# Optimization experiments

Hardware: AMD Instinct MI355X
Metric: run time of the kernel (lower is better)

## Reference

```python
import jax, jax.numpy as jnp
import numpy as np

B, N, I, O, R = 8, 1024, 256, 256, 8


def setup_inputs() -> dict:
    key = jax.random.key(0)
    k1, k2, k3 = jax.random.split(key, 3)
    x = jax.random.normal(k1, (B, N, I), dtype=jnp.float32)
    adj = jax.random.uniform(k2, (B, N, N, R), dtype=jnp.float32)  # soft adjacency [b, src, dst, r]
    weight = jax.random.normal(k3, (R, I, O), dtype=jnp.float32)   # per-relation transform
    return {"x": x, "adj": adj, "weight": weight}


def reference(x, adj, weight):
    # per-relation transformed features: [b, src, r, o]
    f = jnp.einsum('bni,rio->bnro', x, weight)
    # contraction over source nodes and relations, weighted by soft adjacency:
    # out[b, dst, o] = sum_{src, r} adj[b, src, dst, r] * f[b, src, r, o]
    out = jnp.einsum('bnro,bnmr->bmo', f, adj)
    # normalization: total incoming soft-edge weight per destination node
    denom = jnp.clip(adj.sum(axis=(1, 3)), 1e-16, None)  # [b, dst]
    return out / denom[..., None]
```

## Files before the change

kernel.cpp:

```cpp
#include <hip/hip_runtime.h>
#include <hip/hip_bf16.h>
#include <stdint.h>


typedef float          floatx4  __attribute__((ext_vector_type(4)));
typedef short          shortx8  __attribute__((ext_vector_type(8)));
typedef unsigned short ushortx4 __attribute__((ext_vector_type(4)));
typedef unsigned short ushortx8 __attribute__((ext_vector_type(8)));

__device__ __forceinline__ unsigned short f2bf(float f) {
  __hip_bfloat16 h = __float2bfloat16(f);
  unsigned short u; __builtin_memcpy(&u, &h, 2);
  return u;
}

__device__ __forceinline__ void gload16(const void* g, void* l) {
  __builtin_amdgcn_global_load_lds((__attribute__((address_space(1))) void*)g,
                                   (__attribute__((address_space(3))) void*)l,
                                   16, 0, 0);
}

__global__ __launch_bounds__(256) void prep_xw(const float* __restrict__ x,
                                               const float* __restrict__ w,
                                               unsigned short* __restrict__ xbf,
                                               unsigned short* __restrict__ wt) {
  int bid = blockIdx.x;
  if (bid < 1024) {
    int t = bid * 256 + threadIdx.x;
    const float4* p = (const float4*)x + (size_t)t * 2;
    float4 a = p[0], b4 = p[1];
    ushortx8 o;
    o[0] = f2bf(a.x);  o[1] = f2bf(a.y);  o[2] = f2bf(a.z);  o[3] = f2bf(a.w);
    o[4] = f2bf(b4.x); o[5] = f2bf(b4.y); o[6] = f2bf(b4.z); o[7] = f2bf(b4.w);
    *(ushortx8*)(xbf + (size_t)t * 8) = o;
  } else {
    int id = (bid - 1024) * 256 + threadIdx.x;
    int r = id >> 16, i = (id >> 8) & 255, o = id & 255;
    float v = w[((size_t)(r * 256 + i) << 8) + o];
    wt[((size_t)(o * 8 + r) << 8) + i] = f2bf(v);
  }
}

__global__ __launch_bounds__(256) void k1_gemm(const unsigned short* __restrict__ xbf,
                                               const unsigned short* __restrict__ wt,
                                               unsigned short* __restrict__ ft) {
  int bid = blockIdx.x;
  int p0 = (bid & 15) * 128, q0 = (bid >> 4) * 128;
  int l = threadIdx.x & 63, w = threadIdx.x >> 6;
  int lr = l & 15, lg = l >> 4;
  int pw = p0 + (w >> 1) * 64, qw = q0 + (w & 1) * 64;

  floatx4 acc[4][4] = {};
#pragma unroll
  for (int ks = 0; ks < 8; ++ks) {
    shortx8 a[4], b[4];
#pragma unroll
    for (int pi = 0; pi < 4; ++pi)
      a[pi] = *(const shortx8*)(wt + (size_t)(pw + pi * 16 + lr) * 256 + ks * 32 + lg * 8);
#pragma unroll
    for (int qi = 0; qi < 4; ++qi)
      b[qi] = *(const shortx8*)(xbf + (size_t)(qw + qi * 16 + lr) * 256 + ks * 32 + lg * 8);
#pragma unroll
    for (int pi = 0; pi < 4; ++pi)
#pragma unroll
      for (int qi = 0; qi < 4; ++qi)
        acc[pi][qi] = __builtin_amdgcn_mfma_f32_16x16x32_bf16(a[pi], b[qi], acc[pi][qi], 0, 0, 0);
  }
#pragma unroll
  for (int pi = 0; pi < 4; ++pi) {
    int nbase = pw + pi * 16 + lg * 4;
    int o = nbase >> 3, rb = nbase & 7;
#pragma unroll
    for (int qi = 0; qi < 4; ++qi) {
      int m = qw + qi * 16 + lr;
      int b8 = m >> 10, src = m & 1023;
      ushortx4 h;
      h[0] = f2bf(acc[pi][qi][0]); h[1] = f2bf(acc[pi][qi][1]);
      h[2] = f2bf(acc[pi][qi][2]); h[3] = f2bf(acc[pi][qi][3]);
      *(ushortx4*)(ft + ((size_t)(b8 * 256 + o) << 13) + src * 8 + rb) = h;
    }
  }
}

#define ASZ 4096
#define BSZ (128 * 64)
__global__ __launch_bounds__(512, 4) void k2_gemm(const float* __restrict__ adj,
                                                  const unsigned short* __restrict__ ft,
                                                  float* __restrict__ pout,
                                                  float* __restrict__ dpart) {
  __shared__ __align__(16) unsigned short Alds[2 * ASZ];
  __shared__ __align__(16) unsigned short Blds[4 * BSZ];

  int bid = blockIdx.x;
  int b = bid & 7;
  int o0 = ((bid >> 3) & 1) * 128;
  int kc = (bid >> 4) & 1;
  int dst0 = (bid >> 5) * 64;

  int t = threadIdx.x, l = t & 63, w = t >> 6;
  int lr = l & 15, lg = l >> 4;
  int wm = w >> 2, wo = w & 3;

  int dst_l = (t >> 1) & 63;
  int rh = (t & 1) * 4;
  int sA = t >> 7;
  int csw = (l & 7) ^ (l >> 3);

  const size_t adj_b = (size_t)b << 23;
  const unsigned short* ftb = ft + ((size_t)b << 21);
  const int src_base = kc * 512;

  float dsum = 0.f;
  floatx4 acc[2][2] = {};
  float4 avA[2], avB[2];

  auto A_load = [&](int kt, float4* v) {
#pragma unroll
    for (int j = 0; j < 2; ++j) {
      int src = src_base + kt * 8 + sA + j * 4;
      v[j] = *(const float4*)(adj + adj_b + ((size_t)src << 13)
                              + ((size_t)(dst0 + dst_l) << 3) + rh);
    }
  };
  auto A_store = [&](int abuf, const float4* v) {
#pragma unroll
    for (int j = 0; j < 2; ++j) {
      int src_l = sA + j * 4;
      float4 q = v[j];
      dsum += q.x + q.y + q.z + q.w;
      ushortx4 h;
      h[0] = f2bf(q.x); h[1] = f2bf(q.y); h[2] = f2bf(q.z); h[3] = f2bf(q.w);
      int slot = src_l ^ (dst_l & 7);
      *(ushortx4*)&Alds[abuf * ASZ + dst_l * 64 + slot * 8 + rh] = h;
    }
  };
  auto B_stage = [&](int kt, int buf) {
    int kbase = (src_base + kt * 8) * 8;
#pragma unroll
    for (int i = 0; i < 2; ++i) {
      int orow = w * 16 + i * 8 + (l >> 3);
      const unsigned short* g = ftb + ((size_t)(o0 + orow) << 13) + kbase + (csw << 3);
      gload16(g, &Blds[buf * BSZ + (w * 16 + i * 8) * 64]);
    }
  };
  auto compute = [&](int bbuf, int abuf) {
#pragma unroll
    for (int s = 0; s < 2; ++s) {
      int slotbase = s * 4 + lg;
      shortx8 af[2], bfr[2];
#pragma unroll
      for (int mi = 0; mi < 2; ++mi) {
        int arow = wm * 32 + mi * 16 + lr;
        af[mi] = *(const shortx8*)&Alds[abuf * ASZ + arow * 64 + ((slotbase ^ (arow & 7)) << 3)];
      }
#pragma unroll
      for (int ni = 0; ni < 2; ++ni) {
        int brow = wo * 32 + ni * 16 + lr;
        bfr[ni] = *(const shortx8*)&Blds[bbuf * BSZ + brow * 64 + ((slotbase ^ (brow & 7)) << 3)];
      }
#pragma unroll
      for (int mi = 0; mi < 2; ++mi)
#pragma unroll
        for (int ni = 0; ni < 2; ++ni)
          acc[mi][ni] = __builtin_amdgcn_mfma_f32_16x16x32_bf16(af[mi], bfr[ni], acc[mi][ni], 0, 0, 0);
    }
  };

#define STEP(kt, CUR, STG, ABN, ABC, AVx, ISS, STA, FN)                \
  {                                                                    \
    if (ISS) B_stage((kt) + 3, STG);                                   \
    if (STA) A_store(ABN, AVx);                                        \
    if (ISS) A_load((kt) + 3, AVx);                                    \
    compute(CUR, ABC);                                                 \
    if (FN >= 0) {                                                     \
      __builtin_amdgcn_sched_barrier(0);                               \
      if (FN == 8)      asm volatile("s_waitcnt vmcnt(8) lgkmcnt(0)" ::: "memory"); \
      else if (FN == 4) asm volatile("s_waitcnt vmcnt(4) lgkmcnt(0)" ::: "memory"); \
      else              asm volatile("s_waitcnt vmcnt(0) lgkmcnt(0)" ::: "memory"); \
      __builtin_amdgcn_s_barrier();                                    \
      __builtin_amdgcn_sched_barrier(0);                               \
    }                                                                  \
  }

  B_stage(0, 0);
  B_stage(1, 1);
  B_stage(2, 2);
  A_load(0, avA);
  A_store(0, avA);
  A_load(1, avA);
  A_load(2, avB);
  asm volatile("s_waitcnt vmcnt(0) lgkmcnt(0)" ::: "memory");
  __builtin_amdgcn_s_barrier();
  __builtin_amdgcn_sched_barrier(0);

  for (int kt0 = 0; kt0 < 60; kt0 += 4) {
    STEP(kt0 + 0, 0, 3, 1, 0, avA, 1, 1, 8);
    STEP(kt0 + 1, 1, 0, 0, 1, avB, 1, 1, 8);
    STEP(kt0 + 2, 2, 1, 1, 0, avA, 1, 1, 8);
    STEP(kt0 + 3, 3, 2, 0, 1, avB, 1, 1, 8);
  }
  STEP(60, 0, 3, 1, 0, avA, 1, 1, 8);
  STEP(61, 1, 0, 0, 1, avB, 0, 1, 4);
  STEP(62, 2, 0, 1, 0, avA, 0, 1, 0);
  STEP(63, 3, 0, 0, 1, avB, 0, 0, -1);
#undef STEP
  __syncthreads();

  float* dsf = (float*)Alds;
  dsf[t] = dsum;
  __syncthreads();
  if (t < 64) {
    float s = 0.f;
#pragma unroll
    for (int sl = 0; sl < 4; ++sl) {
      s += dsf[sl * 128 + t * 2];
      s += dsf[sl * 128 + t * 2 + 1];
    }
    dpart[kc * 8192 + (b << 10) + dst0 + t] = s;
  }

#pragma unroll
  for (int mi = 0; mi < 2; ++mi) {
#pragma unroll
    for (int reg = 0; reg < 4; ++reg) {
      int row = dst0 + wm * 32 + mi * 16 + lg * 4 + reg;
#pragma unroll
      for (int ni = 0; ni < 2; ++ni) {
        int col = o0 + wo * 32 + ni * 16 + lr;
        pout[(size_t)kc * 2097152 + (((size_t)b << 10) + row) * 256 + col] = acc[mi][ni][reg];
      }
    }
  }
}

__global__ __launch_bounds__(256) void k3_reduce(const float* __restrict__ pout,
                                                 const float* __restrict__ dpart,
                                                 float* __restrict__ outp) {
  int bid = blockIdx.x;
  size_t base = (size_t)bid * 256 + threadIdx.x;
  float v = pout[base] + pout[2097152 + base];
  float d = dpart[bid] + dpart[8192 + bid];
  outp[base] = v / fmaxf(d, 1e-16f);
}

extern "C" void kernel_launch(void* const* d_in, const int* in_sizes, int n_in,
                              void* d_out, int out_size, void* d_ws, size_t ws_size,
                              hipStream_t stream) {
  const float* x   = (const float*)d_in[0];
  const float* adj = (const float*)d_in[1];
  const float* w   = (const float*)d_in[2];
  float* out = (float*)d_out;

  char* ws = (char*)d_ws;
  unsigned short* ft  = (unsigned short*)(ws);
  unsigned short* xbf = (unsigned short*)(ws + 33554432);
  unsigned short* wt  = (unsigned short*)(ws + 37748736);
  float* pout  = (float*)(ws + 38797312);
  float* dpart = (float*)(ws + 55574528);

  prep_xw<<<3072, 256, 0, stream>>>(x, w, xbf, wt);
  k1_gemm<<<1024, 256, 0, stream>>>(xbf, wt, ft);
  k2_gemm<<<512, 512, 0, stream>>>(adj, ft, pout, dpart);
  k3_reduce<<<8192, 256, 0, stream>>>(pout, dpart, out);
}
```

Before: 134.1 us.

## Load k2 B fragments directly into registers and halve destination tile

The aggregation GEMM no longer stages ft tiles through LDS with global_load_lds. Each wave now loads its B fragments straight from global memory into registers, double-buffered one step ahead. The block shrinks to 256 threads covering 32 destination rows, so the grid doubles to 1024 blocks, and the adjacency A tile keeps a three-deep register pipeline with two LDS buffers. This saves LDS capacity and barrier traffic, but B fragments are no longer shared across waves, so ft global reads double and each global load sits on the critical path with less prefetch depth.

After: 215.7 us. +60.9%, slower.

```diff
diff --git a/kernel.cpp b/kernel.cpp
--- a/kernel.cpp
+++ b/kernel.cpp
@@ -12,12 +12,6 @@
   __hip_bfloat16 h = __float2bfloat16(f);
   unsigned short u; __builtin_memcpy(&u, &h, 2);
   return u;
-}
-
-__device__ __forceinline__ void gload16(const void* g, void* l) {
-  __builtin_amdgcn_global_load_lds((__attribute__((address_space(1))) void*)g,
-                                   (__attribute__((address_space(3))) void*)l,
-                                   16, 0, 0);
 }
 
 __global__ __launch_bounds__(256) void prep_xw(const float* __restrict__ x,
@@ -82,37 +76,35 @@
   }
 }
 
-#define ASZ 4096
-#define BSZ (128 * 64)
-__global__ __launch_bounds__(512, 4) void k2_gemm(const float* __restrict__ adj,
+#define ASZ (32 * 64)
+__global__ __launch_bounds__(256, 4) void k2_gemm(const float* __restrict__ adj,
                                                   const unsigned short* __restrict__ ft,
                                                   float* __restrict__ pout,
                                                   float* __restrict__ dpart) {
   __shared__ __align__(16) unsigned short Alds[2 * ASZ];
-  __shared__ __align__(16) unsigned short Blds[4 * BSZ];
 
   int bid = blockIdx.x;
   int b = bid & 7;
   int o0 = ((bid >> 3) & 1) * 128;
   int kc = (bid >> 4) & 1;
-  int dst0 = (bid >> 5) * 64;
+  int dst0 = (bid >> 5) * 32;
 
   int t = threadIdx.x, l = t & 63, w = t >> 6;
   int lr = l & 15, lg = l >> 4;
-  int wm = w >> 2, wo = w & 3;
-
-  int dst_l = (t >> 1) & 63;
-  int rh = (t & 1) * 4;
-  int sA = t >> 7;
-  int csw = (l & 7) ^ (l >> 3);
-
+  bool wq0 = (w == 0);
+
+  const int src_base = kc * 512;
   const size_t adj_b = (size_t)b << 23;
   const unsigned short* ftb = ft + ((size_t)b << 21);
-  const int src_base = kc * 512;
+
+  int dst_l = (t >> 1) & 31;
+  int rh = (t & 1) * 4;
+  int sA = t >> 6;
 
   float dsum = 0.f;
   floatx4 acc[2][2] = {};
-  float4 avA[2], avB[2];
+  float4 a0[2], a1[2], a2[2];
+  shortx8 bs0[2][2], bs1[2][2];
 
   auto A_load = [&](int kt, float4* v) {
 #pragma unroll
@@ -134,87 +126,80 @@
       *(ushortx4*)&Alds[abuf * ASZ + dst_l * 64 + slot * 8 + rh] = h;
     }
   };
-  auto B_stage = [&](int kt, int buf) {
+  auto B_load = [&](int kt, shortx8 (&v)[2][2]) {
     int kbase = (src_base + kt * 8) * 8;
 #pragma unroll
-    for (int i = 0; i < 2; ++i) {
-      int orow = w * 16 + i * 8 + (l >> 3);
-      const unsigned short* g = ftb + ((size_t)(o0 + orow) << 13) + kbase + (csw << 3);
-      gload16(g, &Blds[buf * BSZ + (w * 16 + i * 8) * 64]);
-    }
-  };
-  auto compute = [&](int bbuf, int abuf) {
+    for (int ni = 0; ni < 2; ++ni)
+#pragma unroll
+      for (int s = 0; s < 2; ++s) {
+        int orow = o0 + w * 32 + ni * 16 + lr;
+        v[ni][s] = *(const shortx8*)(ftb + ((size_t)orow << 13) + kbase + (s * 4 + lg) * 8);
+      }
+  };
+  auto compute = [&](int abuf, shortx8 (&bv)[2][2]) {
 #pragma unroll
     for (int s = 0; s < 2; ++s) {
       int slotbase = s * 4 + lg;
-      shortx8 af[2], bfr[2];
+      shortx8 af[2];
 #pragma unroll
       for (int mi = 0; mi < 2; ++mi) {
-        int arow = wm * 32 + mi * 16 + lr;
+        int arow = mi * 16 + lr;
         af[mi] = *(const shortx8*)&Alds[abuf * ASZ + arow * 64 + ((slotbase ^ (arow & 7)) << 3)];
       }
 #pragma unroll
-      for (int ni = 0; ni < 2; ++ni) {
-        int brow = wo * 32 + ni * 16 + lr;
-        bfr[ni] = *(const shortx8*)&Blds[bbuf * BSZ + brow * 64 + ((slotbase ^ (brow & 7)) << 3)];
-      }
-#pragma unroll
       for (int mi = 0; mi < 2; ++mi)
 #pragma unroll
         for (int ni = 0; ni < 2; ++ni)
-          acc[mi][ni] = __builtin_amdgcn_mfma_f32_16x16x32_bf16(af[mi], bfr[ni], acc[mi][ni], 0, 0, 0);
-    }
-  };
-
-#define STEP(kt, CUR, STG, ABN, ABC, AVx, ISS, STA, FN)                \
+          acc[mi][ni] = __builtin_amdgcn_mfma_f32_16x16x32_bf16(af[mi], bv[ni][s], acc[mi][ni], 0, 0, 0);
+    }
+  };
+
+#define STEP(kt, CUR, NXT, ALD, AST, BLD, BCP, ISSA, ISSB, STA, BAR)   \
   {                                                                    \
-    if (ISS) B_stage((kt) + 3, STG);                                   \
-    if (STA) A_store(ABN, AVx);                                        \
-    if (ISS) A_load((kt) + 3, AVx);                                    \
-    compute(CUR, ABC);                                                 \
-    if (FN >= 0) {                                                     \
-      __builtin_amdgcn_sched_barrier(0);                               \
-      if (FN == 8)      asm volatile("s_waitcnt vmcnt(8) lgkmcnt(0)" ::: "memory"); \
-      else if (FN == 4) asm volatile("s_waitcnt vmcnt(4) lgkmcnt(0)" ::: "memory"); \
-      else              asm volatile("s_waitcnt vmcnt(0) lgkmcnt(0)" ::: "memory"); \
+    if (ISSA) A_load((kt) + 3, ALD);                                   \
+    if (ISSB) B_load((kt) + 1, BLD);                                   \
+    if (STA) A_store(NXT, AST);                                        \
+    compute(CUR, BCP);                                                 \
+    if (BAR) {                                                         \
+      asm volatile("s_waitcnt lgkmcnt(0)" ::: "memory");               \
       __builtin_amdgcn_s_barrier();                                    \
-      __builtin_amdgcn_sched_barrier(0);                               \
+      asm volatile("" ::: "memory");                                   \
     }                                                                  \
   }
 
-  B_stage(0, 0);
-  B_stage(1, 1);
-  B_stage(2, 2);
-  A_load(0, avA);
-  A_store(0, avA);
-  A_load(1, avA);
-  A_load(2, avB);
-  asm volatile("s_waitcnt vmcnt(0) lgkmcnt(0)" ::: "memory");
+  A_load(0, a0);
+  A_load(1, a1);
+  A_load(2, a2);
+  B_load(0, bs0);
+  A_store(0, a0);
+  asm volatile("s_waitcnt lgkmcnt(0)" ::: "memory");
   __builtin_amdgcn_s_barrier();
-  __builtin_amdgcn_sched_barrier(0);
-
-  for (int kt0 = 0; kt0 < 60; kt0 += 4) {
-    STEP(kt0 + 0, 0, 3, 1, 0, avA, 1, 1, 8);
-    STEP(kt0 + 1, 1, 0, 0, 1, avB, 1, 1, 8);
-    STEP(kt0 + 2, 2, 1, 1, 0, avA, 1, 1, 8);
-    STEP(kt0 + 3, 3, 2, 0, 1, avB, 1, 1, 8);
-  }
-  STEP(60, 0, 3, 1, 0, avA, 1, 1, 8);
-  STEP(61, 1, 0, 0, 1, avB, 0, 1, 4);
-  STEP(62, 2, 0, 1, 0, avA, 0, 1, 0);
-  STEP(63, 3, 0, 0, 1, avB, 0, 0, -1);
+  asm volatile("" ::: "memory");
+
+  for (int kt0 = 0; kt0 < 60; kt0 += 6) {
+    STEP(kt0 + 0, 0, 1, a0, a1, bs1, bs0, 1, 1, 1, 1);
+    STEP(kt0 + 1, 1, 0, a1, a2, bs0, bs1, 1, 1, 1, 1);
+    STEP(kt0 + 2, 0, 1, a2, a0, bs1, bs0, 1, 1, 1, 1);
+    STEP(kt0 + 3, 1, 0, a0, a1, bs0, bs1, 1, 1, 1, 1);
+    STEP(kt0 + 4, 0, 1, a1, a2, bs1, bs0, 1, 1, 1, 1);
+    STEP(kt0 + 5, 1, 0, a2, a0, bs0, bs1, 1, 1, 1, 1);
+  }
+  STEP(60, 0, 1, a0, a1, bs1, bs0, 1, 1, 1, 1);
+  STEP(61, 1, 0, a1, a2, bs0, bs1, 0, 1, 1, 1);
+  STEP(62, 0, 1, a2, a0, bs1, bs0, 0, 1, 1, 1);
+  STEP(63, 1, 0, a0, a1, bs0, bs1, 0, 0, 0, 0);
 #undef STEP
   __syncthreads();
 
   float* dsf = (float*)Alds;
   dsf[t] = dsum;
   __syncthreads();
-  if (t < 64) {
+  if (t < 32) {
     float s = 0.f;
 #pragma unroll
     for (int sl = 0; sl < 4; ++sl) {
-      s += dsf[sl * 128 + t * 2];
-      s += dsf[sl * 128 + t * 2 + 1];
+      s += dsf[sl * 64 + t * 2];
+      s += dsf[sl * 64 + t * 2 + 1];
     }
     dpart[kc * 8192 + (b << 10) + dst0 + t] = s;
   }
@@ -223,10 +208,10 @@
   for (int mi = 0; mi < 2; ++mi) {
 #pragma unroll
     for (int reg = 0; reg < 4; ++reg) {
-      int row = dst0 + wm * 32 + mi * 16 + lg * 4 + reg;
+      int row = dst0 + mi * 16 + lg * 4 + reg;
 #pragma unroll
       for (int ni = 0; ni < 2; ++ni) {
-        int col = o0 + wo * 32 + ni * 16 + lr;
+        int col = o0 + w * 32 + ni * 16 + lr;
         pout[(size_t)kc * 2097152 + (((size_t)b << 10) + row) * 256 + col] = acc[mi][ni][reg];
       }
     }
@@ -260,6 +245,6 @@
 
   prep_xw<<<3072, 256, 0, stream>>>(x, w, xbf, wt);
   k1_gemm<<<1024, 256, 0, stream>>>(xbf, wt, ft);
-  k2_gemm<<<512, 512, 0, stream>>>(adj, ft, pout, dpart);
+  k2_gemm<<<1024, 256, 0, stream>>>(adj, ft, pout, dpart);
   k3_reduce<<<8192, 256, 0, stream>>>(pout, dpart, out);
 }
```

## Fuse split-K reduction and normalization into k2 via last-arriver atomic flags

Applied to the files above, without the earlier changes.

Removes the separate k3 reduce kernel. Each k2 block writes its partial, then atomically increments a per-tile counter. The second block to finish reads the peer's partial output and denominator and writes the normalized final result. This saves one kernel launch and a full pass over the partials, but adds a memset launch, threadfences, and still writes both partials.

New measurement: 356.3 us. 2.66x slower.

```diff
diff --git a/kernel.cpp b/kernel.cpp
--- a/kernel.cpp
+++ b/kernel.cpp
@@ -87,15 +87,19 @@
 __global__ __launch_bounds__(512, 4) void k2_gemm(const float* __restrict__ adj,
                                                   const unsigned short* __restrict__ ft,
                                                   float* __restrict__ pout,
-                                                  float* __restrict__ dpart) {
+                                                  float* __restrict__ dpart,
+                                                  int* __restrict__ flags,
+                                                  float* __restrict__ outp) {
   __shared__ __align__(16) unsigned short Alds[2 * ASZ];
   __shared__ __align__(16) unsigned short Blds[4 * BSZ];
+  __shared__ int sflag;
 
   int bid = blockIdx.x;
   int b = bid & 7;
   int o0 = ((bid >> 3) & 1) * 128;
   int kc = (bid >> 4) & 1;
   int dst0 = (bid >> 5) * 64;
+  int tileid = (bid & 15) | ((bid >> 5) << 4);
 
   int t = threadIdx.x, l = t & 63, w = t >> 6;
   int lr = l & 15, lg = l >> 4;
@@ -216,8 +220,10 @@
       s += dsf[sl * 128 + t * 2];
       s += dsf[sl * 128 + t * 2 + 1];
     }
+    dsf[512 + t] = s;
     dpart[kc * 8192 + (b << 10) + dst0 + t] = s;
   }
+  __syncthreads();
 
 #pragma unroll
   for (int mi = 0; mi < 2; ++mi) {
@@ -231,16 +237,31 @@
       }
     }
   }
-}
-
-__global__ __launch_bounds__(256) void k3_reduce(const float* __restrict__ pout,
-                                                 const float* __restrict__ dpart,
-                                                 float* __restrict__ outp) {
-  int bid = blockIdx.x;
-  size_t base = (size_t)bid * 256 + threadIdx.x;
-  float v = pout[base] + pout[2097152 + base];
-  float d = dpart[bid] + dpart[8192 + bid];
-  outp[base] = v / fmaxf(d, 1e-16f);
+
+  __threadfence();
+  if (t == 0) sflag = atomicAdd(&flags[tileid], 1);
+  __syncthreads();
+  if (sflag == 1) {
+    __threadfence();
+    int kp = 1 - kc;
+#pragma unroll
+    for (int mi = 0; mi < 2; ++mi) {
+#pragma unroll
+      for (int reg = 0; reg < 4; ++reg) {
+        int rl = wm * 32 + mi * 16 + lg * 4 + reg;
+        int row = dst0 + rl;
+        float d = dsf[512 + rl] + dpart[kp * 8192 + (b << 10) + row];
+        float dinv = 1.f / fmaxf(d, 1e-16f);
+#pragma unroll
+        for (int ni = 0; ni < 2; ++ni) {
+          int col = o0 + wo * 32 + ni * 16 + lr;
+          size_t idx = (((size_t)b << 10) + row) * 256 + col;
+          float v = acc[mi][ni][reg] + pout[(size_t)kp * 2097152 + idx];
+          outp[idx] = v * dinv;
+        }
+      }
+    }
+  }
 }
 
 extern "C" void kernel_launch(void* const* d_in, const int* in_sizes, int n_in,
@@ -257,9 +278,10 @@
   unsigned short* wt  = (unsigned short*)(ws + 37748736);
   float* pout  = (float*)(ws + 38797312);
   float* dpart = (float*)(ws + 55574528);
-
+  int*   flags = (int*)(ws + 55640064);
+
+  hipMemsetAsync(flags, 0, 256 * sizeof(int), stream);
   prep_xw<<<3072, 256, 0, stream>>>(x, w, xbf, wt);
   k1_gemm<<<1024, 256, 0, stream>>>(xbf, wt, ft);
-  k2_gemm<<<512, 512, 0, stream>>>(adj, ft, pout, dpart);
-  k3_reduce<<<8192, 256, 0, stream>>>(pout, dpart, out);
-}
+  k2_gemm<<<512, 512, 0, stream>>>(adj, ft, pout, dpart, flags, out);
+}
```
